# Optimization experiments

Hardware: AMD Instinct MI355X
Metric: run time of the kernel (lower is better)

Reference implementation:

```python
import jax, jax.numpy as jnp
import numpy as np

B, N, DIN, DOUT, DA = 8, 2048, 128, 128, 2
NEG_SLOPE = 0.2


def setup_inputs() -> dict:
    key = jax.random.key(0)
    k = jax.random.split(key, 7)
    x = jax.random.normal(k[0], (B, N, DIN), dtype=jnp.float32)
    mask = jax.random.randint(k[1], (B, N, N), 0, 2, dtype=jnp.int32)
    s = 1.0 / np.sqrt(DIN)
    Wr = jax.random.uniform(k[2], (DA, DIN), jnp.float32, -s, s)      # linear_row.weight
    Wc = jax.random.uniform(k[3], (DA, DIN), jnp.float32, -s, s)      # linear_col.weight
    sa = 1.0 / np.sqrt(2 * DA)
    Wcat = jax.random.uniform(k[4], (2 * DA,), jnp.float32, -sa, sa)  # linear_concat.weight [1, 2*DA] flattened
    Wx = jax.random.uniform(k[5], (DOUT, DIN), jnp.float32, -s, s)    # linear_x.weight
    bx = jax.random.uniform(k[6], (DOUT,), jnp.float32, -s, s)        # linear_x.bias
    return {"x": x, "mask": mask, "Wr": Wr, "Wc": Wc, "Wcat": Wcat, "Wx": Wx, "bx": bx}


def reference(x, mask, Wr, Wc, Wcat, Wx, bx):
    # Row/col projections to tiny attention dim: [B, N, DA]
    row = jnp.einsum('bnd,ad->bna', x, Wr)
    col = jnp.einsum('bnd,ad->bna', x, Wc)
    # Concat scoring: e_ij = linear_concat(LeakyReLU(cat(row_i, col_j)))
    # decomposes as a1 . LR(row_i) + a2 . LR(col_j) -- avoids materializing [B,N,N,2*DA]
    a1, a2 = Wcat[:DA], Wcat[DA:]
    lr_row = jax.nn.leaky_relu(row, NEG_SLOPE) @ a1   # [B, N]
    lr_col = jax.nn.leaky_relu(col, NEG_SLOPE) @ a2   # [B, N]
    e = lr_row[:, :, None] + lr_col[:, None, :]       # [B, N, N]
    # Masked softmax over columns j
    e = jnp.where(mask > 0, e, jnp.float32(-1e9))
    atten = jax.nn.softmax(e, axis=-1)                # [B, N, N]
    # Value projection + combine
    xv = jnp.einsum('bnd,od->bno', x, Wx) + bx        # [B, N, DOUT]
    out = jnp.einsum('bij,bjo->bio', atten, xv)       # [B, N, DOUT]
    return out
```

## Files before the change

### kernel.cpp

```cpp
#include <hip/hip_runtime.h>


typedef __bf16 bf16x8 __attribute__((ext_vector_type(8)));
typedef __bf16 bf16x4 __attribute__((ext_vector_type(4)));
typedef float  f32x4  __attribute__((ext_vector_type(4)));
typedef int    i32x4  __attribute__((ext_vector_type(4)));
typedef unsigned int u32;

#define MFMA_BF16(a, b, c) __builtin_amdgcn_mfma_f32_16x16x32_bf16((a), (b), (c), 0, 0, 0)

#define GLOAD_LDS16(gp, lp)                                                     \
  __builtin_amdgcn_global_load_lds(                                             \
      (const __attribute__((address_space(1))) void*)(gp),                      \
      (__attribute__((address_space(3))) void*)(lp), 16, 0, 0)

static __device__ __forceinline__ bf16x8 cvt8(f32x4 a, f32x4 b) {
  bf16x8 r;
  r[0] = (__bf16)a[0]; r[1] = (__bf16)a[1]; r[2] = (__bf16)a[2]; r[3] = (__bf16)a[3];
  r[4] = (__bf16)b[0]; r[5] = (__bf16)b[1]; r[6] = (__bf16)b[2]; r[7] = (__bf16)b[3];
  return r;
}

__global__ __launch_bounds__(256) void prep_kernel(
    const float* __restrict__ x, const float* __restrict__ Wc,
    const float* __restrict__ Wcat, const float* __restrict__ Wx,
    const float* __restrict__ bx, __bf16* __restrict__ u,
    __bf16* __restrict__ wcol)
{
  __shared__ __bf16 lds[8192];
  const int blk = blockIdx.x;
  const int b = blk >> 5, mt = blk & 31;
  const int wv = threadIdx.x >> 6, lane = threadIdx.x & 63;
  const int np = lane & 15, G = lane >> 4;
  const int r0 = mt * 64 + wv * 16;

  const float* xp = x + ((size_t)(b * 2048 + r0 + np)) * 128 + G * 8;
  bf16x8 af[4];
#pragma unroll
  for (int kk = 0; kk < 4; ++kk) {
    f32x4 x0 = *(const f32x4*)(xp + kk * 32);
    f32x4 x1 = *(const f32x4*)(xp + kk * 32 + 4);
    af[kk] = cvt8(x0, x1);
  }

  f32x4 acc[8], accC;
#pragma unroll
  for (int n = 0; n < 8; ++n) { acc[n][0] = 0.f; acc[n][1] = 0.f; acc[n][2] = 0.f; acc[n][3] = 0.f; }
  accC[0] = accC[1] = accC[2] = accC[3] = 0.f;

#pragma unroll
  for (int n = 0; n < 8; ++n) {
    const float* wp = Wx + (n * 16 + np) * 128 + G * 8;
#pragma unroll
    for (int kk = 0; kk < 4; ++kk) {
      f32x4 w0 = *(const f32x4*)(wp + kk * 32);
      f32x4 w1 = *(const f32x4*)(wp + kk * 32 + 4);
      acc[n] = MFMA_BF16(af[kk], cvt8(w0, w1), acc[n]);
    }
  }
#pragma unroll
  for (int kk = 0; kk < 4; ++kk) {
    bf16x8 bf;
    if (np < 2) {
      const float* cp = Wc + np * 128 + kk * 32 + G * 8;
      f32x4 c0 = *(const f32x4*)cp;
      f32x4 c1 = *(const f32x4*)(cp + 4);
      bf = cvt8(c0, c1);
    } else {
#pragma unroll
      for (int j = 0; j < 8; ++j) bf[j] = (__bf16)0.0f;
    }
    accC = MFMA_BF16(af[kk], bf, accC);
  }

  const float a20 = Wcat[2], a21 = Wcat[3];
  float wexp[4];
#pragma unroll
  for (int r = 0; r < 4; ++r) {
    float c0 = __shfl(accC[r], lane & 48);
    float c1 = __shfl(accC[r], (lane & 48) | 1);
    c0 = c0 > 0.f ? c0 : 0.2f * c0;
    c1 = c1 > 0.f ? c1 : 0.2f * c1;
    wexp[r] = __expf(c0 * a20 + c1 * a21);
  }
  if (np == 0) {
    bf16x4 w4;
#pragma unroll
    for (int r = 0; r < 4; ++r) w4[r] = (__bf16)wexp[r];
    *(bf16x4*)(wcol + (size_t)b * 2048 + r0 + 4 * G) = w4;
  }

  const int t_rel = wv >> 1;
  const int g_store = (wv & 1) * 2 + (G >> 1);
  const int j0 = (G & 1) * 4;
#pragma unroll
  for (int n = 0; n < 8; ++n) {
    float bxv = bx[n * 16 + np];
    bf16x4 v;
#pragma unroll
    for (int r = 0; r < 4; ++r) v[r] = (__bf16)(wexp[r] * (acc[n][r] + bxv));
    *(bf16x4*)(&lds[(t_rel * 8 + n) * 512 + g_store * 128 + np * 8 + j0]) = v;
  }
  __syncthreads();
  __bf16* dst = u + ((size_t)(b * 64 + mt * 2)) * 4096;
#pragma unroll
  for (int it = 0; it < 4; ++it) {
    int s = it * 256 + threadIdx.x;
    ((i32x4*)dst)[s] = ((const i32x4*)lds)[s];
  }
}

__global__ __launch_bounds__(256) void attn_kernel(
    const int* __restrict__ mask, const __bf16* __restrict__ u,
    const __bf16* __restrict__ wcol, float* __restrict__ out)
{
  __shared__ char smem[4 * 12288 + 4096];
  char* wbuf = smem + 49152;
  const int b = blockIdx.x & 7, rt = blockIdx.x >> 3;
  const int wv = threadIdx.x >> 6, lane = threadIdx.x & 63;
  const int np = lane & 15, G = lane >> 4;
  const int row0 = rt * 32;
  const int n0 = wv * 2, n1 = n0 + 1;
  const int swzB = (np & 7) << 4;

  const char* gmask = (const char*)(mask + ((size_t)b * 2048 + row0) * 2048);
  const char* gu    = (const char*)u + (size_t)b * 64 * 8192;
  const char* gw    = (const char*)(wcol + (size_t)b * 2048);

  const int srow = lane >> 3;
  const long long moff = (size_t)(8 * wv + srow) * 8192 + (((lane & 7) ^ srow) << 4);

  f32x4 acc[2][2];
#pragma unroll
  for (int mi = 0; mi < 2; ++mi)
#pragma unroll
    for (int n = 0; n < 2; ++n) { acc[mi][n][0] = 0.f; acc[mi][n][1] = 0.f; acc[mi][n][2] = 0.f; acc[mi][n][3] = 0.f; }
  float den[2] = {0.f, 0.f};

#define STAGE(it, nb)                                                          \
  do {                                                                         \
    char* mb_ = smem + (nb) * 12288;                                           \
    GLOAD_LDS16(gmask + moff + (it) * 128, mb_ + wv * 1024);                   \
    const char* up_ = gu + (size_t)(it) * 8192 + lane * 16;                    \
    GLOAD_LDS16(up_ + (2 * wv) * 1024, mb_ + 4096 + (2 * wv) * 1024);          \
    GLOAD_LDS16(up_ + (2 * wv + 1) * 1024, mb_ + 4096 + (2 * wv + 1) * 1024);  \
  } while (0)

#define CONSUME(it, nb)                                                        \
  do {                                                                         \
    const char* mb = smem + (nb) * 12288;                                      \
    const char* ub = mb + 4096;                                                \
    bf16x8 W = *(const bf16x8*)(wbuf + (it) * 64 + G * 16);                    \
    float wf[8];                                                               \
    _Pragma("unroll")                                                          \
    for (int j = 0; j < 8; ++j) wf[j] = (float)W[j];                           \
    bf16x8 U0 = *(const bf16x8*)(ub + n0 * 1024 + lane * 16);                  \
    bf16x8 U1 = *(const bf16x8*)(ub + n1 * 1024 + lane * 16);                  \
    _Pragma("unroll")                                                          \
    for (int mi = 0; mi < 2; ++mi) {                                           \
      const char* rp = mb + (mi * 16 + np) * 128;                              \
      i32x4 ma = *(const i32x4*)(rp + ((G * 32) ^ swzB));                      \
      i32x4 mz = *(const i32x4*)(rp + ((G * 32 + 16) ^ swzB));                 \
      union { u32 w[4]; bf16x8 v; } A;                                         \
      A.w[0] = (ma[0] ? 0x3F80u : 0u) | (ma[1] ? 0x3F800000u : 0u);            \
      A.w[1] = (ma[2] ? 0x3F80u : 0u) | (ma[3] ? 0x3F800000u : 0u);            \
      A.w[2] = (mz[0] ? 0x3F80u : 0u) | (mz[1] ? 0x3F800000u : 0u);            \
      A.w[3] = (mz[2] ? 0x3F80u : 0u) | (mz[3] ? 0x3F800000u : 0u);            \
      float d = den[mi];                                                       \
      d += ma[0] ? wf[0] : 0.f; d += ma[1] ? wf[1] : 0.f;                      \
      d += ma[2] ? wf[2] : 0.f; d += ma[3] ? wf[3] : 0.f;                      \
      d += mz[0] ? wf[4] : 0.f; d += mz[1] ? wf[5] : 0.f;                      \
      d += mz[2] ? wf[6] : 0.f; d += mz[3] ? wf[7] : 0.f;                      \
      den[mi] = d;                                                             \
      acc[mi][0] = MFMA_BF16(A.v, U0, acc[mi][0]);                             \
      acc[mi][1] = MFMA_BF16(A.v, U1, acc[mi][1]);                             \
    }                                                                          \
  } while (0)

  GLOAD_LDS16(gw + wv * 1024 + lane * 16, wbuf + wv * 1024);
  STAGE(0, 0); STAGE(1, 1); STAGE(2, 2);

  for (int it = 0; it <= 61; ++it) {
    asm volatile("s_waitcnt vmcnt(6)" ::: "memory");
    __builtin_amdgcn_s_barrier();
    CONSUME(it, it & 3);
    if (it <= 60) STAGE(it + 3, (it + 3) & 3);
  }
  asm volatile("s_waitcnt vmcnt(3)" ::: "memory");
  __builtin_amdgcn_s_barrier();
  CONSUME(62, 2);
  asm volatile("s_waitcnt vmcnt(0)" ::: "memory");
  __builtin_amdgcn_s_barrier();
  CONSUME(63, 3);
#undef STAGE
#undef CONSUME

#pragma unroll
  for (int mi = 0; mi < 2; ++mi) {
    float dr = den[mi] + __shfl_xor(den[mi], 16);
    dr += __shfl_xor(dr, 32);
#pragma unroll
    for (int r = 0; r < 4; ++r) {
      float dv = __shfl(dr, 4 * G + r);
      float inv = 1.0f / dv;
      float* op = out + ((size_t)b * 2048 + row0 + mi * 16 + 4 * G + r) * 128 + np;
      op[n0 * 16] = acc[mi][0][r] * inv;
      op[n1 * 16] = acc[mi][1][r] * inv;
    }
  }
}

extern "C" void kernel_launch(void* const* d_in, const int* in_sizes, int n_in,
                              void* d_out, int out_size, void* d_ws, size_t ws_size,
                              hipStream_t stream) {
  const float* x    = (const float*)d_in[0];
  const int*   mask = (const int*)d_in[1];
  const float* Wc   = (const float*)d_in[3];
  const float* Wcat = (const float*)d_in[4];
  const float* Wx   = (const float*)d_in[5];
  const float* bx   = (const float*)d_in[6];
  float* out = (float*)d_out;

  const size_t U_BYTES = (size_t)8 * 64 * 4096 * 2;
  if (ws_size < U_BYTES + 8 * 2048 * 2) return;
  __bf16* u    = (__bf16*)d_ws;
  __bf16* wcol = (__bf16*)((char*)d_ws + U_BYTES);

  prep_kernel<<<256, 256, 0, stream>>>(x, Wc, Wcat, Wx, bx, u, wcol);
  attn_kernel<<<512, 256, 0, stream>>>(mask, u, wcol, out);
}
```

Measured before the change: 232.1 us.

## Pack int32 mask into bitmask in separate kernel before attention

Adds a pack_kernel that reads the int32 mask once and compresses it into per-tile bitmasks via wave ballots. The attention kernel then loads the compact bits up front instead of streaming 4-byte mask values per column tile, which shrinks LDS staging and the pipeline's load count. The prep kernel's u/wcol layout is reshuffled to match the new column ordering. The full mask is still read once from global memory, so the total HBM traffic is about the same; the change adds a kernel launch and mainly moves mask decoding out of the MFMA loop.

```diff
diff --git a/kernel.cpp b/kernel.cpp
--- a/kernel.cpp
+++ b/kernel.cpp
@@ -2,10 +2,10 @@
 
 
 typedef __bf16 bf16x8 __attribute__((ext_vector_type(8)));
-typedef __bf16 bf16x4 __attribute__((ext_vector_type(4)));
 typedef float  f32x4  __attribute__((ext_vector_type(4)));
 typedef int    i32x4  __attribute__((ext_vector_type(4)));
 typedef unsigned int u32;
+typedef unsigned long long u64;
 
 #define MFMA_BF16(a, b, c) __builtin_amdgcn_mfma_f32_16x16x32_bf16((a), (b), (c), 0, 0, 0)
 
@@ -83,23 +83,23 @@
     c1 = c1 > 0.f ? c1 : 0.2f * c1;
     wexp[r] = __expf(c0 * a20 + c1 * a21);
   }
+
   if (np == 0) {
-    bf16x4 w4;
-#pragma unroll
-    for (int r = 0; r < 4; ++r) w4[r] = (__bf16)wexp[r];
-    *(bf16x4*)(wcol + (size_t)b * 2048 + r0 + 4 * G) = w4;
+    const int t = mt * 2 + (wv >> 1);
+#pragma unroll
+    for (int r = 0; r < 4; ++r)
+      wcol[(size_t)b * 2048 + t * 32 + r * 8 + 4 * (wv & 1) + G] = (__bf16)wexp[r];
   }
 
   const int t_rel = wv >> 1;
-  const int g_store = (wv & 1) * 2 + (G >> 1);
-  const int j0 = (G & 1) * 4;
+  const int jp = 4 * (wv & 1) + G;
 #pragma unroll
   for (int n = 0; n < 8; ++n) {
     float bxv = bx[n * 16 + np];
-    bf16x4 v;
-#pragma unroll
-    for (int r = 0; r < 4; ++r) v[r] = (__bf16)(wexp[r] * (acc[n][r] + bxv));
-    *(bf16x4*)(&lds[(t_rel * 8 + n) * 512 + g_store * 128 + np * 8 + j0]) = v;
+#pragma unroll
+    for (int r = 0; r < 4; ++r)
+      lds[(t_rel * 8 + n) * 512 + (r * 16 + np) * 8 + jp] =
+          (__bf16)(wexp[r] * (acc[n][r] + bxv));
   }
   __syncthreads();
   __bf16* dst = u + ((size_t)(b * 64 + mt * 2)) * 4096;
@@ -110,25 +110,48 @@
   }
 }
 
+__global__ __launch_bounds__(256) void pack_kernel(
+    const int* __restrict__ mask, u32* __restrict__ bits)
+{
+  const int b = blockIdx.x & 7, rt = blockIdx.x >> 3;
+  const int wv = threadIdx.x >> 6, lane = threadIdx.x & 63;
+  const int* mbase = mask + ((size_t)b * 2048 + rt * 32) * 2048;
+  u32* obase = bits + (size_t)(b * 64 + rt) * 2048;
+  const int sh = (lane & 7) * 8;
+
+  for (int r8 = 0; r8 < 8; ++r8) {
+    const int row = wv * 8 + r8;
+    const int* rp = mbase + (size_t)row * 2048;
+#pragma unroll
+    for (int c = 0; c < 8; ++c) {
+      i32x4 v = *(const i32x4*)(rp + c * 256 + lane * 4);
+      u64 b0 = __ballot(v[0] != 0);
+      u64 b1 = __ballot(v[1] != 0);
+      u64 b2 = __ballot(v[2] != 0);
+      u64 b3 = __ballot(v[3] != 0);
+      u32 d = (u32)((b0 >> sh) & 0xFF) | ((u32)((b1 >> sh) & 0xFF) << 8) |
+              ((u32)((b2 >> sh) & 0xFF) << 16) | ((u32)((b3 >> sh) & 0xFF) << 24);
+      if (lane < 8) obase[(c * 8 + lane) * 32 + row] = d;
+    }
+  }
+}
+
 __global__ __launch_bounds__(256) void attn_kernel(
-    const int* __restrict__ mask, const __bf16* __restrict__ u,
-    const __bf16* __restrict__ wcol, float* __restrict__ out)
+    const __bf16* __restrict__ u, const __bf16* __restrict__ wcol,
+    const u32* __restrict__ bits, float* __restrict__ out)
 {
-  __shared__ char smem[4 * 12288 + 4096];
-  char* wbuf = smem + 49152;
+  __shared__ char smem[4 * 8192 + 8192 + 4096];
+  char* bitlds = smem + 32768;
+  char* wlds = smem + 40960;
   const int b = blockIdx.x & 7, rt = blockIdx.x >> 3;
   const int wv = threadIdx.x >> 6, lane = threadIdx.x & 63;
   const int np = lane & 15, G = lane >> 4;
   const int row0 = rt * 32;
   const int n0 = wv * 2, n1 = n0 + 1;
-  const int swzB = (np & 7) << 4;
-
-  const char* gmask = (const char*)(mask + ((size_t)b * 2048 + row0) * 2048);
-  const char* gu    = (const char*)u + (size_t)b * 64 * 8192;
-  const char* gw    = (const char*)(wcol + (size_t)b * 2048);
-
-  const int srow = lane >> 3;
-  const long long moff = (size_t)(8 * wv + srow) * 8192 + (((lane & 7) ^ srow) << 4);
+
+  const char* gu = (const char*)u + (size_t)b * 64 * 8192;
+  const char* gw = (const char*)(wcol + (size_t)b * 2048);
+  const char* gbits = (const char*)(bits + (size_t)(b * 64 + rt) * 2048);
 
   f32x4 acc[2][2];
 #pragma unroll
@@ -139,18 +162,16 @@
 
 #define STAGE(it, nb)                                                          \
   do {                                                                         \
-    char* mb_ = smem + (nb) * 12288;                                           \
-    GLOAD_LDS16(gmask + moff + (it) * 128, mb_ + wv * 1024);                   \
-    const char* up_ = gu + (size_t)(it) * 8192 + lane * 16;                    \
-    GLOAD_LDS16(up_ + (2 * wv) * 1024, mb_ + 4096 + (2 * wv) * 1024);          \
-    GLOAD_LDS16(up_ + (2 * wv + 1) * 1024, mb_ + 4096 + (2 * wv + 1) * 1024);  \
+    char* dst = smem + (nb) * 8192;                                            \
+    const char* src = gu + (size_t)(it) * 8192 + lane * 16;                    \
+    GLOAD_LDS16(src + (2 * wv) * 1024, dst + (2 * wv) * 1024);                 \
+    GLOAD_LDS16(src + (2 * wv + 1) * 1024, dst + (2 * wv + 1) * 1024);         \
   } while (0)
 
 #define CONSUME(it, nb)                                                        \
   do {                                                                         \
-    const char* mb = smem + (nb) * 12288;                                      \
-    const char* ub = mb + 4096;                                                \
-    bf16x8 W = *(const bf16x8*)(wbuf + (it) * 64 + G * 16);                    \
+    const char* ub = smem + (nb) * 8192;                                       \
+    bf16x8 W = *(const bf16x8*)(wlds + (it) * 64 + G * 16);                    \
     float wf[8];                                                               \
     _Pragma("unroll")                                                          \
     for (int j = 0; j < 8; ++j) wf[j] = (float)W[j];                           \
@@ -158,35 +179,38 @@
     bf16x8 U1 = *(const bf16x8*)(ub + n1 * 1024 + lane * 16);                  \
     _Pragma("unroll")                                                          \
     for (int mi = 0; mi < 2; ++mi) {                                           \
-      const char* rp = mb + (mi * 16 + np) * 128;                              \
-      i32x4 ma = *(const i32x4*)(rp + ((G * 32) ^ swzB));                      \
-      i32x4 mz = *(const i32x4*)(rp + ((G * 32 + 16) ^ swzB));                 \
+      u32 m8 = (u32)(unsigned char)bitlds[(it) * 128 + (mi * 16 + np) * 4 + G];\
       union { u32 w[4]; bf16x8 v; } A;                                         \
-      A.w[0] = (ma[0] ? 0x3F80u : 0u) | (ma[1] ? 0x3F800000u : 0u);            \
-      A.w[1] = (ma[2] ? 0x3F80u : 0u) | (ma[3] ? 0x3F800000u : 0u);            \
-      A.w[2] = (mz[0] ? 0x3F80u : 0u) | (mz[1] ? 0x3F800000u : 0u);            \
-      A.w[3] = (mz[2] ? 0x3F80u : 0u) | (mz[3] ? 0x3F800000u : 0u);            \
+      A.w[0] = ((m8 & 1u) ? 0x3F80u : 0u) | ((m8 & 2u) ? 0x3F800000u : 0u);    \
+      A.w[1] = ((m8 & 4u) ? 0x3F80u : 0u) | ((m8 & 8u) ? 0x3F800000u : 0u);    \
+      A.w[2] = ((m8 & 16u) ? 0x3F80u : 0u) | ((m8 & 32u) ? 0x3F800000u : 0u);  \
+      A.w[3] = ((m8 & 64u) ? 0x3F80u : 0u) | ((m8 & 128u) ? 0x3F800000u : 0u); \
       float d = den[mi];                                                       \
-      d += ma[0] ? wf[0] : 0.f; d += ma[1] ? wf[1] : 0.f;                      \
-      d += ma[2] ? wf[2] : 0.f; d += ma[3] ? wf[3] : 0.f;                      \
-      d += mz[0] ? wf[4] : 0.f; d += mz[1] ? wf[5] : 0.f;                      \
-      d += mz[2] ? wf[6] : 0.f; d += mz[3] ? wf[7] : 0.f;                      \
+      d += (m8 & 1u) ? wf[0] : 0.f;  d += (m8 & 2u) ? wf[1] : 0.f;             \
+      d += (m8 & 4u) ? wf[2] : 0.f;  d += (m8 & 8u) ? wf[3] : 0.f;             \
+      d += (m8 & 16u) ? wf[4] : 0.f; d += (m8 & 32u) ? wf[5] : 0.f;            \
+      d += (m8 & 64u) ? wf[6] : 0.f; d += (m8 & 128u) ? wf[7] : 0.f;           \
       den[mi] = d;                                                             \
       acc[mi][0] = MFMA_BF16(A.v, U0, acc[mi][0]);                             \
       acc[mi][1] = MFMA_BF16(A.v, U1, acc[mi][1]);                             \
     }                                                                          \
   } while (0)
 
-  GLOAD_LDS16(gw + wv * 1024 + lane * 16, wbuf + wv * 1024);
+  GLOAD_LDS16(gbits + (2 * wv) * 1024 + lane * 16, bitlds + (2 * wv) * 1024);
+  GLOAD_LDS16(gbits + (2 * wv + 1) * 1024 + lane * 16, bitlds + (2 * wv + 1) * 1024);
+  GLOAD_LDS16(gw + wv * 1024 + lane * 16, wlds + wv * 1024);
   STAGE(0, 0); STAGE(1, 1); STAGE(2, 2);
 
-  for (int it = 0; it <= 61; ++it) {
-    asm volatile("s_waitcnt vmcnt(6)" ::: "memory");
+  for (int it = 0; it <= 60; ++it) {
+    asm volatile("s_waitcnt vmcnt(4)" ::: "memory");
     __builtin_amdgcn_s_barrier();
     CONSUME(it, it & 3);
-    if (it <= 60) STAGE(it + 3, (it + 3) & 3);
-  }
-  asm volatile("s_waitcnt vmcnt(3)" ::: "memory");
+    STAGE(it + 3, (it + 3) & 3);
+  }
+  asm volatile("s_waitcnt vmcnt(4)" ::: "memory");
+  __builtin_amdgcn_s_barrier();
+  CONSUME(61, 1);
+  asm volatile("s_waitcnt vmcnt(2)" ::: "memory");
   __builtin_amdgcn_s_barrier();
   CONSUME(62, 2);
   asm volatile("s_waitcnt vmcnt(0)" ::: "memory");
@@ -222,10 +246,14 @@
   float* out = (float*)d_out;
 
   const size_t U_BYTES = (size_t)8 * 64 * 4096 * 2;
-  if (ws_size < U_BYTES + 8 * 2048 * 2) return;
+  const size_t W_BYTES = (size_t)8 * 2048 * 2;
+  const size_t B_BYTES = (size_t)8 * 64 * 2048 * 4;
+  if (ws_size < U_BYTES + W_BYTES + B_BYTES) return;
   __bf16* u    = (__bf16*)d_ws;
   __bf16* wcol = (__bf16*)((char*)d_ws + U_BYTES);
+  u32*    bits = (u32*)((char*)d_ws + U_BYTES + W_BYTES);
 
   prep_kernel<<<256, 256, 0, stream>>>(x, Wc, Wcat, Wx, bx, u, wcol);
-  attn_kernel<<<512, 256, 0, stream>>>(mask, u, wcol, out);
-}
+  pack_kernel<<<512, 256, 0, stream>>>(mask, bits);
+  attn_kernel<<<512, 256, 0, stream>>>(u, wcol, bits, out);
+}
```

New measurement: 272.2 us. 1.17x slower.
